# Kernel tuning notes

Hardware: AMD Instinct MI355X
Metric: run time of the kernel (lower is better)

The kernel has to match this reference:

```python
import jax, jax.numpy as jnp
import numpy as np

CUTOFF = 5.0       # module __init__ arg
BOX_L = 40.0       # side of cubic region positions are drawn from (OBC: no box passed)
N_ATOMS = 8192
MAX_PAIRS = 1_048_576  # static bound on directed pairs (expected ~550k)


def setup_inputs() -> dict:
    key = jax.random.key(0)
    positions = jax.random.uniform(key, (N_ATOMS, 3), dtype=jnp.float32) * BOX_L
    return {"positions": positions}


def _pairwise_dist(x):
    # Euclidean distance matrix via the gram trick (avoids [N,N,3] intermediate).
    sq = jnp.sum(x * x, axis=1)
    d2 = sq[:, None] + sq[None, :] - 2.0 * (x @ x.T)
    return jnp.sqrt(jnp.maximum(d2, 0.0))


def _safe_norm(dr):
    # norm with zero-safe gradient (padded pairs have dr == 0)
    d2 = jnp.sum(dr * dr, axis=1)
    ok = d2 > 0
    return jnp.where(ok, jnp.sqrt(jnp.where(ok, d2, 1.0)), 0.0)


def reference(positions):
    n = positions.shape[0]
    dist = _pairwise_dist(positions)                      # [N, N]
    mask = (dist < CUTOFF) & (~jnp.eye(n, dtype=bool))    # exclude self-pairs
    # torch.argwhere equivalent, padded to static size; padding -> (0, 0)
    i, j = jnp.nonzero(mask, size=MAX_PAIRS, fill_value=0)
    pairs = jnp.stack([i, j], axis=1).astype(jnp.int32)   # [MAX_PAIRS, 2]
    # pairs_buffer_scales: 1 where i < j else 0 (padding (0,0) -> 0)
    buffer_scales = (i < j).astype(jnp.int32)
    # pairs_ds (pbc_flag=False): ||r_j - r_i||
    dr = positions[j] - positions[i]                      # [MAX_PAIRS, 3]
    ds = _safe_norm(dr)
    return pairs, buffer_scales, ds
```

## Files before the change

### kernel.cpp

```cpp
#include <hip/hip_runtime.h>

#define MAXP 1048576
#define NATOMS 8192
#define D2_CUT 0x1.8ffffep+4f
#define CINV 0.175f
#define CAP 192

#define W_SORTPOS 0
#define W_SORTID  32768
#define W_ROWCNT  36864
#define W_ROWOFF  45056
#define W_CELLOFF 53248

__device__ __forceinline__ float sq3_nc(float x, float y, float z) {
#pragma clang fp contract(off)
  float a = x * x;
  float b = y * y;
  float c = z * z;
  return (a + b) + c;
}

__device__ __forceinline__ float d2_gram(float xi, float yi, float zi, float sqi,
                                         float xj, float yj, float zj, float sqj) {
#pragma clang fp contract(off)
  float g = xi * xj;
  g = __builtin_fmaf(yi, yj, g);
  g = __builtin_fmaf(zi, zj, g);
  float t = sqi + sqj;
  float d2 = t - 2.0f * g;
  return d2;
}

__device__ __forceinline__ float d2_direct(float xi, float yi, float zi,
                                           float xj, float yj, float zj) {
#pragma clang fp contract(off)
  float dx = xj - xi;
  float dy = yj - yi;
  float dz = zj - zi;
  float a = dx * dx;
  float b = dy * dy;
  float c = dz * dz;
  return (a + b) + c;
}

__device__ __forceinline__ int cellco(float v) {
  int c = (int)(v * CINV);
  return c < 0 ? 0 : (c > 6 ? 6 : c);
}

__global__ __launch_bounds__(256) void nl_pack(float* __restrict__ out) {
  const int gtid = blockIdx.x * 256 + threadIdx.x;
  float4* o4 = (float4*)out;
#pragma unroll
  for (int k = 0; k < 16; ++k)
    o4[k * 65536 + gtid] = make_float4(0.f, 0.f, 0.f, 0.f);
}

__global__ __launch_bounds__(1024) void nl_prep(const float* __restrict__ pos,
                                                float* __restrict__ ws) {
  __shared__ int hcnt[343];
  __shared__ int hoff[344];
  __shared__ int hcur[343];
  __shared__ int s[512];
  const int tid = threadIdx.x;
  if (tid < 343) { hcnt[tid] = 0; hcur[tid] = 0; }
  __syncthreads();

  float x[8], y[8], z[8];
  int cl[8];
#pragma unroll
  for (int k = 0; k < 8; ++k) {
    int a = tid + k * 1024;
    x[k] = pos[3 * a]; y[k] = pos[3 * a + 1]; z[k] = pos[3 * a + 2];
    cl[k] = cellco(x[k]) + 7 * cellco(y[k]) + 49 * cellco(z[k]);
    atomicAdd(&hcnt[cl[k]], 1);
  }
  __syncthreads();

  if (tid < 512) s[tid] = (tid < 343) ? hcnt[tid] : 0;
  __syncthreads();
  for (int off = 1; off < 512; off <<= 1) {
    int v = (tid < 512 && tid >= off) ? s[tid - off] : 0;
    __syncthreads();
    if (tid < 512) s[tid] += v;
    __syncthreads();
  }
  if (tid < 343) hoff[tid] = (tid == 0) ? 0 : s[tid - 1];
  if (tid == 343) hoff[343] = NATOMS;
  __syncthreads();
  if (tid < 344) ((int*)(ws + W_CELLOFF))[tid] = hoff[tid];

  unsigned short* sortid = (unsigned short*)(ws + W_SORTID);
  float4* sortpos = (float4*)(ws + W_SORTPOS);
#pragma unroll
  for (int k = 0; k < 8; ++k) {
    int slot = hoff[cl[k]] + atomicAdd(&hcur[cl[k]], 1);
    sortid[slot] = (unsigned short)(tid + k * 1024);
    sortpos[slot] = make_float4(x[k], y[k], z[k], sq3_nc(x[k], y[k], z[k]));
  }
}

__global__ __launch_bounds__(256, 8) void nl_count(float* __restrict__ ws) {
  const int lane = threadIdx.x & 63;
  const int wave = threadIdx.x >> 6;
  const int slot = blockIdx.x * 4 + wave;

  const float4* __restrict__ sp4 = (const float4*)(ws + W_SORTPOS);
  const unsigned short* __restrict__ sid = (const unsigned short*)(ws + W_SORTID);
  const int* __restrict__ celloff = (const int*)(ws + W_CELLOFF);
  int* rowcnt = (int*)(ws + W_ROWCNT);

  const float4 pi = sp4[slot];
  int cx = cellco(pi.x), cy = cellco(pi.y), cz = cellco(pi.z);
  int x0 = max(cx - 1, 0), x1 = min(cx + 1, 6);
  int y0 = max(cy - 1, 0), y1 = min(cy + 1, 6);
  int z0 = max(cz - 1, 0), z1 = min(cz + 1, 6);

  int cnt = 0;
  for (int icz = z0; icz <= z1; ++icz)
    for (int icy = y0; icy <= y1; ++icy) {
      int cb = 7 * icy + 49 * icz;
      int st = celloff[cb + x0];
      int en = celloff[cb + x1 + 1];
      for (int bb = st; bb < en; bb += 64) {
        int t = bb + lane;
        bool v = t < en;
        int t2 = v ? t : (en - 1);
        float4 p = sp4[t2];
        float d2 = d2_gram(pi.x, pi.y, pi.z, pi.w, p.x, p.y, p.z, p.w);
        cnt += (v && d2 < D2_CUT) ? 1 : 0;
      }
    }
  for (int off = 32; off > 0; off >>= 1) cnt += __shfl_down(cnt, off, 64);
  if (lane == 0) rowcnt[sid[slot]] = cnt - 1;
}

__global__ __launch_bounds__(1024) void nl_rowscan(float* __restrict__ ws) {
  const int* cnts = (const int*)(ws + W_ROWCNT);
  int* offs = (int*)(ws + W_ROWOFF);
  __shared__ int s[1024];
  const int tid = threadIdx.x;
  const int base = tid * 8;
  int local[8];
  int sum = 0;
#pragma unroll
  for (int k = 0; k < 8; ++k) { local[k] = sum; sum += cnts[base + k]; }
  s[tid] = sum;
  __syncthreads();
  for (int off = 1; off < 1024; off <<= 1) {
    int v = (tid >= off) ? s[tid - off] : 0;
    __syncthreads();
    s[tid] += v;
    __syncthreads();
  }
  int excl = (tid == 0) ? 0 : s[tid - 1];
#pragma unroll
  for (int k = 0; k < 8; ++k) offs[base + k] = excl + local[k];
}

__global__ __launch_bounds__(256, 8) void nl_write(const float* __restrict__ pos,
                                                   float* __restrict__ out,
                                                   const float* __restrict__ ws) {
  __shared__ unsigned int bmap[4][256];
  __shared__ unsigned short stj[4][CAP];
  const int lane = threadIdx.x & 63;
  const int wave = threadIdx.x >> 6;
  const int slot = blockIdx.x * 4 + wave;

  const float4* __restrict__ sp4 = (const float4*)(ws + W_SORTPOS);
  const unsigned short* __restrict__ sid = (const unsigned short*)(ws + W_SORTID);
  const int* __restrict__ celloff = (const int*)(ws + W_CELLOFF);
  const int* __restrict__ rowoff = (const int*)(ws + W_ROWOFF);

#pragma unroll
  for (int q = 0; q < 4; ++q) bmap[wave][lane + 64 * q] = 0u;

  const float4 pi = sp4[slot];
  const int rid = sid[slot];
  int cx = cellco(pi.x), cy = cellco(pi.y), cz = cellco(pi.z);
  int x0 = max(cx - 1, 0), x1 = min(cx + 1, 6);
  int y0 = max(cy - 1, 0), y1 = min(cy + 1, 6);
  int z0 = max(cz - 1, 0), z1 = min(cz + 1, 6);

  for (int icz = z0; icz <= z1; ++icz)
    for (int icy = y0; icy <= y1; ++icy) {
      int cb = 7 * icy + 49 * icz;
      int st = celloff[cb + x0];
      int en = celloff[cb + x1 + 1];
      for (int bb = st; bb < en; bb += 64) {
        int t = bb + lane;
        bool v = t < en;
        int t2 = v ? t : (en - 1);
        float4 p = sp4[t2];
        int jd = sid[t2];
        float d2 = d2_gram(pi.x, pi.y, pi.z, pi.w, p.x, p.y, p.z, p.w);
        if (v && d2 < D2_CUT)
          atomicOr(&bmap[wave][jd >> 5], 1u << (jd & 31));
      }
    }
  if (lane == 0)
    atomicAnd(&bmap[wave][rid >> 5], ~(1u << (rid & 31)));

  int ktot = 0;
#pragma unroll
  for (int seg = 0; seg < 4; ++seg) {
    int w = seg * 64 + lane;
    unsigned bits = bmap[wave][w];
    int pc = __popc(bits);
    int incl = pc;
    for (int d = 1; d < 64; d <<= 1) {
      int u = __shfl_up(incl, d, 64);
      if (lane >= d) incl += u;
    }
    int bpos = ktot + incl - pc;
    while (bits) {
      int b = __builtin_ctz(bits);
      bits &= bits - 1;
      if (bpos < CAP) stj[wave][bpos] = (unsigned short)(w * 32 + b);
      ++bpos;
    }
    ktot += __shfl(incl, 63, 64);
  }

  int k = ktot > CAP ? CAP : ktot;
  int ro = rowoff[rid];
  for (int s2 = lane; s2 < k; s2 += 64) {
    int j = stj[wave][s2];
    int o = ro + s2;
    if ((unsigned)o < MAXP) {
      float xj = pos[3 * j], yj = pos[3 * j + 1], zj = pos[3 * j + 2];
      float ds = sqrtf(d2_direct(pi.x, pi.y, pi.z, xj, yj, zj));
      ((float2*)out)[o] = make_float2((float)rid, (float)j);
      out[2 * MAXP + o] = (rid < j) ? 1.0f : 0.0f;
      out[3 * MAXP + o] = ds;
    }
  }
}

extern "C" void kernel_launch(void* const* d_in, const int* in_sizes, int n_in,
                              void* d_out, int out_size, void* d_ws, size_t ws_size,
                              hipStream_t stream) {
  const float* pos = (const float*)d_in[0];
  float* out = (float*)d_out;
  float* ws = (float*)d_ws;

  nl_pack<<<256, 256, 0, stream>>>(out);
  nl_prep<<<1, 1024, 0, stream>>>(pos, ws);
  nl_count<<<2048, 256, 0, stream>>>(ws);
  nl_rowscan<<<1, 1024, 0, stream>>>(ws);
  nl_write<<<2048, 256, 0, stream>>>(pos, out, ws);
}
```

Measured before the change: 96.66 us.

## Fuse zero-fill into prep and replace row scan with per-group atomic sums

The output zero-fill is moved into extra blocks of the prep kernel, so it runs alongside the single-block binning. The separate row-scan kernel is dropped: the count kernel atomically accumulates per-64-row group sums, and each write wave rebuilds its row offset from the group sums plus the earlier rows in its own group using a wave reduction. This cuts the launch count from five to three, at the cost of global atomics in the count kernel and extra loads and a reduction at the start of every write wave.

```diff
diff --git a/kernel.cpp b/kernel.cpp
--- a/kernel.cpp
+++ b/kernel.cpp
@@ -9,8 +9,8 @@
 #define W_SORTPOS 0
 #define W_SORTID  32768
 #define W_ROWCNT  36864
-#define W_ROWOFF  45056
-#define W_CELLOFF 53248
+#define W_GRPSUM  45056
+#define W_CELLOFF 45568
 
 __device__ __forceinline__ float sq3_nc(float x, float y, float z) {
 #pragma clang fp contract(off)
@@ -48,21 +48,23 @@
   return c < 0 ? 0 : (c > 6 ? 6 : c);
 }
 
-__global__ __launch_bounds__(256) void nl_pack(float* __restrict__ out) {
-  const int gtid = blockIdx.x * 256 + threadIdx.x;
-  float4* o4 = (float4*)out;
-#pragma unroll
-  for (int k = 0; k < 16; ++k)
-    o4[k * 65536 + gtid] = make_float4(0.f, 0.f, 0.f, 0.f);
-}
-
 __global__ __launch_bounds__(1024) void nl_prep(const float* __restrict__ pos,
+                                                float* __restrict__ out,
                                                 float* __restrict__ ws) {
+  const int tid = threadIdx.x;
+  if (blockIdx.x != 0) {
+    float4* o4 = (float4*)out;
+    const int b = blockIdx.x - 1;
+    for (int i = b * 1024 + tid; i < 1048576; i += 63 * 1024)
+      o4[i] = make_float4(0.f, 0.f, 0.f, 0.f);
+    if (blockIdx.x == 1 && tid < 512) ((int*)(ws + W_GRPSUM))[tid] = 0;
+    return;
+  }
+
   __shared__ int hcnt[343];
   __shared__ int hoff[344];
   __shared__ int hcur[343];
   __shared__ int s[512];
-  const int tid = threadIdx.x;
   if (tid < 343) { hcnt[tid] = 0; hcur[tid] = 0; }
   __syncthreads();
 
@@ -109,6 +111,7 @@
   const unsigned short* __restrict__ sid = (const unsigned short*)(ws + W_SORTID);
   const int* __restrict__ celloff = (const int*)(ws + W_CELLOFF);
   int* rowcnt = (int*)(ws + W_ROWCNT);
+  int* grpsum = (int*)(ws + W_GRPSUM);
 
   const float4 pi = sp4[slot];
   int cx = cellco(pi.x), cy = cellco(pi.y), cz = cellco(pi.z);
@@ -132,30 +135,11 @@
       }
     }
   for (int off = 32; off > 0; off >>= 1) cnt += __shfl_down(cnt, off, 64);
-  if (lane == 0) rowcnt[sid[slot]] = cnt - 1;
-}
-
-__global__ __launch_bounds__(1024) void nl_rowscan(float* __restrict__ ws) {
-  const int* cnts = (const int*)(ws + W_ROWCNT);
-  int* offs = (int*)(ws + W_ROWOFF);
-  __shared__ int s[1024];
-  const int tid = threadIdx.x;
-  const int base = tid * 8;
-  int local[8];
-  int sum = 0;
-#pragma unroll
-  for (int k = 0; k < 8; ++k) { local[k] = sum; sum += cnts[base + k]; }
-  s[tid] = sum;
-  __syncthreads();
-  for (int off = 1; off < 1024; off <<= 1) {
-    int v = (tid >= off) ? s[tid - off] : 0;
-    __syncthreads();
-    s[tid] += v;
-    __syncthreads();
-  }
-  int excl = (tid == 0) ? 0 : s[tid - 1];
-#pragma unroll
-  for (int k = 0; k < 8; ++k) offs[base + k] = excl + local[k];
+  if (lane == 0) {
+    const int rid = sid[slot];
+    rowcnt[rid] = cnt - 1;
+    atomicAdd(&grpsum[rid >> 6], cnt - 1);
+  }
 }
 
 __global__ __launch_bounds__(256, 8) void nl_write(const float* __restrict__ pos,
@@ -170,13 +154,22 @@
   const float4* __restrict__ sp4 = (const float4*)(ws + W_SORTPOS);
   const unsigned short* __restrict__ sid = (const unsigned short*)(ws + W_SORTID);
   const int* __restrict__ celloff = (const int*)(ws + W_CELLOFF);
-  const int* __restrict__ rowoff = (const int*)(ws + W_ROWOFF);
+  const int* __restrict__ rowcnt = (const int*)(ws + W_ROWCNT);
+  const int* __restrict__ grpsum = (const int*)(ws + W_GRPSUM);
 
 #pragma unroll
   for (int q = 0; q < 4; ++q) bmap[wave][lane + 64 * q] = 0u;
 
   const float4 pi = sp4[slot];
   const int rid = sid[slot];
+
+  const int G = rid >> 6;
+  int pre = ((lane < G) ? grpsum[lane] : 0) +
+            ((lane + 64 < G) ? grpsum[lane + 64] : 0) +
+            ((lane < (rid & 63)) ? rowcnt[(rid & ~63) + lane] : 0);
+  for (int off = 32; off > 0; off >>= 1) pre += __shfl_down(pre, off, 64);
+  const int ro = __shfl(pre, 0, 64);
+
   int cx = cellco(pi.x), cy = cellco(pi.y), cz = cellco(pi.z);
   int x0 = max(cx - 1, 0), x1 = min(cx + 1, 6);
   int y0 = max(cy - 1, 0), y1 = min(cy + 1, 6);
@@ -223,7 +216,6 @@
   }
 
   int k = ktot > CAP ? CAP : ktot;
-  int ro = rowoff[rid];
   for (int s2 = lane; s2 < k; s2 += 64) {
     int j = stj[wave][s2];
     int o = ro + s2;
@@ -244,9 +236,7 @@
   float* out = (float*)d_out;
   float* ws = (float*)d_ws;
 
-  nl_pack<<<256, 256, 0, stream>>>(out);
-  nl_prep<<<1, 1024, 0, stream>>>(pos, ws);
+  nl_prep<<<64, 1024, 0, stream>>>(pos, out, ws);
   nl_count<<<2048, 256, 0, stream>>>(ws);
-  nl_rowscan<<<1, 1024, 0, stream>>>(ws);
   nl_write<<<2048, 256, 0, stream>>>(pos, out, ws);
 }
```

Result: slower. 105.2 us (+8.8%).
